# Performance work log

Hardware: AMD Instinct MI355X
Metric: run time of the kernel (lower is better)

Reference implementation:

```python
import jax, jax.numpy as jnp
import numpy as np


def _conv(x, k, pad):
    # x: [B,1,H,W], k: [1,1,kh,kw]
    return jax.lax.conv_general_dilated(
        x, k, window_strides=(1, 1), padding=[(pad, pad), (pad, pad)],
        dimension_numbers=('NCHW', 'OIHW', 'NCHW'))


def _gauss_kernel(size=15, sigma=2.0):
    c = np.arange(size, dtype=np.float32) - size // 2
    k = np.exp(-(c[:, None] ** 2 + c[None, :] ** 2) / (2.0 * sigma ** 2))
    k = k / k.sum()
    return jnp.asarray(k, dtype=jnp.float32)[None, None]


_SOBEL_X = jnp.array([[[[-1., 0., 1.], [-2., 0., 2.], [-1., 0., 1.]]]], dtype=jnp.float32)
_SOBEL_Y = jnp.array([[[[-1., -2., -1.], [0., 0., 0.], [1., 2., 1.]]]], dtype=jnp.float32)
_GAUSS = _gauss_kernel(15, 2.0)


def _edge_density(img):
    gray = 0.299 * img[:, 0] + 0.587 * img[:, 1] + 0.114 * img[:, 2]  # [B,H,W]
    box = jnp.ones((1, 1, 5, 5), jnp.float32) / 25.0  # avg_pool2d, count_include_pad
    blurred = _conv(gray[:, None], box, 2)
    gx = _conv(blurred, _SOBEL_X, 1)
    gy = _conv(blurred, _SOBEL_Y, 1)
    mag = jnp.sqrt(gx ** 2 + gy ** 2)
    hi = mag.max() * 0.2
    lo = hi * 0.3
    edge_map = ((mag > lo) & (mag < hi)).astype(jnp.float32)
    return _conv(edge_map, _GAUSS, 7)  # [B,1,H,W]


def _color_sparsity(img):
    # Replaces the O(K*B*H*W) python loop over unique quantized colors with a
    # 32^3-bin histogram (scatter-add) and a single per-pixel gather.
    b, c, h, w = img.shape
    idx = jnp.clip(jnp.round(img * 31.0), 0, 31).astype(jnp.int32)  # [B,3,H,W]
    code = idx[:, 0] * 1024 + idx[:, 1] * 32 + idx[:, 2]  # [B,H,W]
    counts = jnp.zeros(32 * 32 * 32, jnp.float32).at[code.reshape(-1)].add(1.0)
    prob = counts[code] / float(b * h * w)  # [B,H,W]
    return (-jnp.log(prob + 1e-9) * 1.5)[:, None]  # [B,1,H,W]


def setup_inputs() -> dict:
    key = jax.random.key(0)
    img = jax.random.uniform(key, (1, 3, 3072, 3072), dtype=jnp.float32)
    return {
        'img': img,
        'alpha': jnp.asarray(0.5, dtype=jnp.float32),
        'beta': jnp.asarray(0.5, dtype=jnp.float32),
    }


def reference(img, alpha, beta):
    ed = _edge_density(img)
    cs = _color_sparsity(img)
    en = (ed - ed.min()) / (ed.max() - ed.min() + 1e-9)
    cn = (cs - cs.min()) / (cs.max() - cs.min() + 1e-9)
    return jax.nn.sigmoid(alpha * en + beta * cn)  # [B,1,H,W]
```

## Files before the change

kernel.cpp:

```cpp
#include <hip/hip_runtime.h>
#include <math.h>

#define TW 3072
#define TH 3072
#define NPIX (TW*TH)

__device__ __forceinline__ int qcode(float r, float g, float b) {
    int ir = min(max((int)rintf(__fmul_rn(r, 31.f)), 0), 31);
    int ig = min(max((int)rintf(__fmul_rn(g, 31.f)), 0), 31);
    int ib = min(max((int)rintf(__fmul_rn(b, 31.f)), 0), 31);
    return ir * 1024 + ig * 32 + ib;
}

__device__ __forceinline__ float grayf(float r, float g, float b) {
    return __fadd_rn(__fadd_rn(__fmul_rn(0.299f, r), __fmul_rn(0.587f, g)),
                     __fmul_rn(0.114f, b));
}

__global__ __launch_bounds__(1024) void k_pre(const float4* __restrict__ img4,
                                              float4* __restrict__ gray4,
                                              ushort4* __restrict__ code4,
                                              unsigned* __restrict__ parthist,
                                              unsigned* __restrict__ scal) {
    if (blockIdx.x == 0 && threadIdx.x == 0) {
        scal[0] = 0u;
        scal[1] = 0x7F800000u;
        scal[2] = 0u;
        scal[3] = 0u;
        scal[4] = 0xFFFFFFFFu;
    }
    __shared__ unsigned lh[16384];
    for (int t = threadIdx.x; t < 16384; t += 1024) lh[t] = 0u;
    __syncthreads();
    const int total4 = NPIX / 4;
    const int stride = 256 * 1024;
    int base = blockIdx.x * 1024 + threadIdx.x;
#pragma unroll
    for (int k = 0; k < 8; k += 2) {
        int p = base + k * stride;
        int q = p + stride;
        float4 r0 = img4[p], g0 = img4[p + total4], b0 = img4[p + 2 * total4];
        float4 r1 = img4[q], g1 = img4[q + total4], b1 = img4[q + 2 * total4];
        float4 gy0, gy1;
        gy0.x = grayf(r0.x, g0.x, b0.x); gy0.y = grayf(r0.y, g0.y, b0.y);
        gy0.z = grayf(r0.z, g0.z, b0.z); gy0.w = grayf(r0.w, g0.w, b0.w);
        gy1.x = grayf(r1.x, g1.x, b1.x); gy1.y = grayf(r1.y, g1.y, b1.y);
        gy1.z = grayf(r1.z, g1.z, b1.z); gy1.w = grayf(r1.w, g1.w, b1.w);
        gray4[p] = gy0;
        gray4[q] = gy1;
        int c0 = qcode(r0.x, g0.x, b0.x), c1 = qcode(r0.y, g0.y, b0.y);
        int c2 = qcode(r0.z, g0.z, b0.z), c3 = qcode(r0.w, g0.w, b0.w);
        int d0 = qcode(r1.x, g1.x, b1.x), d1 = qcode(r1.y, g1.y, b1.y);
        int d2 = qcode(r1.z, g1.z, b1.z), d3 = qcode(r1.w, g1.w, b1.w);
        atomicAdd(&lh[c0 >> 1], (c0 & 1) ? 0x10000u : 1u);
        atomicAdd(&lh[c1 >> 1], (c1 & 1) ? 0x10000u : 1u);
        atomicAdd(&lh[c2 >> 1], (c2 & 1) ? 0x10000u : 1u);
        atomicAdd(&lh[c3 >> 1], (c3 & 1) ? 0x10000u : 1u);
        atomicAdd(&lh[d0 >> 1], (d0 & 1) ? 0x10000u : 1u);
        atomicAdd(&lh[d1 >> 1], (d1 & 1) ? 0x10000u : 1u);
        atomicAdd(&lh[d2 >> 1], (d2 & 1) ? 0x10000u : 1u);
        atomicAdd(&lh[d3 >> 1], (d3 & 1) ? 0x10000u : 1u);
        ushort4 cc, dd;
        cc.x = (unsigned short)c0; cc.y = (unsigned short)c1;
        cc.z = (unsigned short)c2; cc.w = (unsigned short)c3;
        dd.x = (unsigned short)d0; dd.y = (unsigned short)d1;
        dd.z = (unsigned short)d2; dd.w = (unsigned short)d3;
        code4[p] = cc;
        code4[q] = dd;
    }
    {
        int p = base + 8 * stride;
        float4 r = img4[p], g = img4[p + total4], b = img4[p + 2 * total4];
        float4 gy;
        gy.x = grayf(r.x, g.x, b.x); gy.y = grayf(r.y, g.y, b.y);
        gy.z = grayf(r.z, g.z, b.z); gy.w = grayf(r.w, g.w, b.w);
        gray4[p] = gy;
        int c0 = qcode(r.x, g.x, b.x), c1 = qcode(r.y, g.y, b.y);
        int c2 = qcode(r.z, g.z, b.z), c3 = qcode(r.w, g.w, b.w);
        atomicAdd(&lh[c0 >> 1], (c0 & 1) ? 0x10000u : 1u);
        atomicAdd(&lh[c1 >> 1], (c1 & 1) ? 0x10000u : 1u);
        atomicAdd(&lh[c2 >> 1], (c2 & 1) ? 0x10000u : 1u);
        atomicAdd(&lh[c3 >> 1], (c3 & 1) ? 0x10000u : 1u);
        ushort4 cc;
        cc.x = (unsigned short)c0; cc.y = (unsigned short)c1;
        cc.z = (unsigned short)c2; cc.w = (unsigned short)c3;
        code4[p] = cc;
    }
    __syncthreads();
    unsigned* dst = parthist + (size_t)blockIdx.x * 16384;
    for (int t = threadIdx.x; t < 16384; t += 1024) dst[t] = lh[t];
}

__global__ void k_reduce(const unsigned* __restrict__ parthist, unsigned* __restrict__ hist,
                         float* __restrict__ cstab, unsigned* __restrict__ scal) {
    int b = blockIdx.x * blockDim.x + threadIdx.x;
    unsigned lo = 0u, hi = 0u;
#pragma unroll 4
    for (int k = 0; k < 256; k++) {
        unsigned v = parthist[(size_t)k * 16384 + b];
        lo += v & 0xFFFFu;
        hi += v >> 16;
    }
    hist[2 * b] = lo;
    hist[2 * b + 1] = hi;
    const float N = (float)NPIX;
    cstab[2 * b]     = -logf((float)lo / N + 1e-9f) * 1.5f;
    cstab[2 * b + 1] = -logf((float)hi / N + 1e-9f) * 1.5f;
    unsigned mx = max(lo, hi);
    unsigned mn = 0xFFFFFFFFu;
    if (lo) mn = lo;
    if (hi) mn = min(mn, hi);
#pragma unroll
    for (int o = 32; o > 0; o >>= 1) {
        mx = max(mx, (unsigned)__shfl_down((int)mx, o));
        mn = min(mn, (unsigned)__shfl_down((int)mn, o));
    }
    __shared__ unsigned smx[4], smn[4];
    int lane = threadIdx.x & 63, wv = threadIdx.x >> 6;
    if (lane == 0) { smx[wv] = mx; smn[wv] = mn; }
    __syncthreads();
    if (threadIdx.x == 0) {
        unsigned a = max(max(smx[0], smx[1]), max(smx[2], smx[3]));
        unsigned c = min(min(smn[0], smn[1]), min(smn[2], smn[3]));
        atomicMax(&scal[3], a);
        atomicMin(&scal[4], c);
    }
}

__device__ __forceinline__ void blockMaxMinAtomic(float vmax, float vmin,
                                                  unsigned* pmax, unsigned* pmin) {
#pragma unroll
    for (int o = 32; o > 0; o >>= 1) {
        vmax = fmaxf(vmax, __shfl_down(vmax, o));
        vmin = fminf(vmin, __shfl_down(vmin, o));
    }
    __shared__ float smax[8], smin[8];
    int lane = threadIdx.x & 63, wv = threadIdx.x >> 6;
    if (lane == 0) { smax[wv] = vmax; smin[wv] = vmin; }
    __syncthreads();
    if (threadIdx.x == 0) {
        int nw = blockDim.x >> 6;
        float a = smax[0], b = smin[0];
        for (int k = 1; k < nw; k++) { a = fmaxf(a, smax[k]); b = fminf(b, smin[k]); }
        if (pmax) atomicMax(pmax, __float_as_uint(a));
        if (pmin) atomicMin(pmin, __float_as_uint(b));
    }
}

#define BS_W 256
#define BS_H 24
#define GTW 264
#define GTH 30
#define BLW 260
#define BLH 26
__global__ __launch_bounds__(512) void k_boxsobel(const float* __restrict__ g,
                                                  float* __restrict__ mag,
                                                  unsigned* __restrict__ scal) {
    __shared__ float GT[GTH * GTW];
    __shared__ float BL[BLH * BLW];
    int tid = threadIdx.x;
    int x0 = blockIdx.x * BS_W;
    int y0 = blockIdx.y * BS_H;
    for (int t = tid; t < GTH * GTW; t += 512) {
        int ly = t / GTW, lx = t - ly * GTW;
        int y = y0 - 3 + ly, x = x0 - 3 + lx;
        GT[t] = ((unsigned)y < TH && (unsigned)x < TW) ? g[(size_t)y * TW + x] : 0.f;
    }
    __syncthreads();
    for (int t = tid; t < BLH * 65; t += 512) {
        int by = t / 65, gx = t - by * 65;
        int c0 = gx * 4;
        float acc[4] = {0.f, 0.f, 0.f, 0.f};
#pragma unroll
        for (int a = 0; a < 5; a++) {
            const float* rp = &GT[(by + a) * GTW + c0];
            float4 A = *(const float4*)rp;
            float4 B = *(const float4*)(rp + 4);
            float v[8] = {A.x, A.y, A.z, A.w, B.x, B.y, B.z, B.w};
#pragma unroll
            for (int j = 0; j < 4; j++)
#pragma unroll
                for (int b = 0; b < 5; b++)
                    acc[j] = __fadd_rn(acc[j], __fmul_rn(v[j + b], 0.04f));
        }
        int yb = y0 - 1 + by;
        float4 o;
        float* ov = (float*)&o;
#pragma unroll
        for (int j = 0; j < 4; j++) {
            int xb = x0 - 1 + c0 + j;
            ov[j] = ((unsigned)yb < TH && (unsigned)xb < TW) ? acc[j] : 0.f;
        }
        *(float4*)&BL[by * BLW + c0] = o;
    }
    __syncthreads();
    float tmax = 0.f;
    for (int t = tid; t < 24 * 64; t += 512) {
        int oy = t >> 6, gx = t & 63;
        int c0 = gx * 4;
        float v[3][6];
#pragma unroll
        for (int a = 0; a < 3; a++) {
            const float* rp = &BL[(oy + a) * BLW + c0];
            float4 P = *(const float4*)rp;
            float2 Q = *(const float2*)(rp + 4);
            v[a][0] = P.x; v[a][1] = P.y; v[a][2] = P.z; v[a][3] = P.w;
            v[a][4] = Q.x; v[a][5] = Q.y;
        }
        float4 mo;
        float* mv = (float*)&mo;
#pragma unroll
        for (int j = 0; j < 4; j++) {
            float gxv = 0.f;
            gxv = __fadd_rn(gxv, __fmul_rn(-1.f, v[0][j + 0]));
            gxv = __fadd_rn(gxv, v[0][j + 2]);
            gxv = __fadd_rn(gxv, __fmul_rn(-2.f, v[1][j + 0]));
            gxv = __fadd_rn(gxv, __fmul_rn(2.f, v[1][j + 2]));
            gxv = __fadd_rn(gxv, __fmul_rn(-1.f, v[2][j + 0]));
            gxv = __fadd_rn(gxv, v[2][j + 2]);
            float gyv = 0.f;
            gyv = __fadd_rn(gyv, __fmul_rn(-1.f, v[0][j + 0]));
            gyv = __fadd_rn(gyv, __fmul_rn(-2.f, v[0][j + 1]));
            gyv = __fadd_rn(gyv, __fmul_rn(-1.f, v[0][j + 2]));
            gyv = __fadd_rn(gyv, v[2][j + 0]);
            gyv = __fadd_rn(gyv, __fmul_rn(2.f, v[2][j + 1]));
            gyv = __fadd_rn(gyv, v[2][j + 2]);
            float m = sqrtf(__fadd_rn(__fmul_rn(gxv, gxv), __fmul_rn(gyv, gyv)));
            mv[j] = m;
            tmax = fmaxf(tmax, m);
        }
        *(float4*)&mag[(size_t)(y0 + oy) * TW + x0 + c0] = mo;
    }
    blockMaxMinAtomic(tmax, 0.f, &scal[0], nullptr);
}

#define GS_W 256
#define GS_H 48
#define E_H 62
#define EWB 10
__global__ __launch_bounds__(512) void k_gauss(const float* __restrict__ mag,
                                               float* __restrict__ ed,
                                               const unsigned* __restrict__ scal,
                                               unsigned* __restrict__ scalw) {
    __shared__ float wt[15];
    __shared__ unsigned E8[E_H * EWB];
    __shared__ float EH[E_H * GS_W];
    if (threadIdx.x == 0) {
        float w[15];
        float s = 0.f;
        for (int t = 0; t < 15; t++) {
            int c = t - 7;
            w[t] = expf(-(float)(c * c) * 0.125f);
            s += w[t];
        }
        for (int t = 0; t < 15; t++) wt[t] = w[t] / s;
    }
    __syncthreads();
    float magmax = __uint_as_float(scal[0]);
    float hi = __fmul_rn(magmax, 0.2f);
    float lo = __fmul_rn(hi, 0.3f);
    int tid = threadIdx.x;
    int lane = tid & 63, wave = tid >> 6;
    int x0 = blockIdx.x * GS_W;
    int y0 = blockIdx.y * GS_H;
    for (int item = wave; item < E_H * 5; item += 8) {
        int ly = item / 5, ch = item - ly * 5;
        int y = y0 - 7 + ly;
        int lx = ch * 64 + lane;
        int x = x0 - 7 + lx;
        float m = ((unsigned)y < TH && lx < 270 && (unsigned)x < TW)
                      ? mag[(size_t)y * TW + x] : 0.f;
        unsigned long long mask = __ballot(m > lo && m < hi);
        if (lane < 2) E8[ly * EWB + ch * 2 + lane] = (unsigned)(mask >> (32 * lane));
    }
    __syncthreads();
    for (int t = tid; t < E_H * 64; t += 512) {
        int ly = t >> 6, gx = t & 63;
        int c0 = gx * 4;
        int w0 = c0 >> 5, sh = c0 & 31;
        unsigned lo32 = E8[ly * EWB + w0];
        unsigned hi32 = E8[ly * EWB + w0 + 1];
        unsigned long long win = (((unsigned long long)hi32 << 32) | lo32) >> sh;
        float e[18];
#pragma unroll
        for (int j = 0; j < 18; j++) e[j] = (float)((unsigned)(win >> j) & 1u);
        float4 o;
        float* ov = (float*)&o;
#pragma unroll
        for (int j = 0; j < 4; j++) {
            float acc = 0.f;
#pragma unroll
            for (int k = 0; k < 15; k++) acc = fmaf(e[j + k], wt[k], acc);
            ov[j] = acc;
        }
        *(float4*)&EH[ly * GS_W + c0] = o;
    }
    __syncthreads();
    float tmin = INFINITY, tmax = 0.f;
    for (int t = tid; t < GS_H * 64; t += 512) {
        int r = t >> 6, gx = t & 63;
        int c0 = gx * 4;
        float a0 = 0.f, a1 = 0.f, a2 = 0.f, a3 = 0.f;
#pragma unroll
        for (int k = 0; k < 15; k++) {
            float4 v = *(const float4*)&EH[(r + k) * GS_W + c0];
            a0 = fmaf(v.x, wt[k], a0);
            a1 = fmaf(v.y, wt[k], a1);
            a2 = fmaf(v.z, wt[k], a2);
            a3 = fmaf(v.w, wt[k], a3);
        }
        float4 o; o.x = a0; o.y = a1; o.z = a2; o.w = a3;
        *(float4*)&ed[(size_t)(y0 + r) * TW + x0 + c0] = o;
        tmin = fminf(tmin, fminf(fminf(a0, a1), fminf(a2, a3)));
        tmax = fmaxf(tmax, fmaxf(fmaxf(a0, a1), fmaxf(a2, a3)));
    }
    blockMaxMinAtomic(tmax, tmin, &scalw[2], &scalw[1]);
}

__global__ void k_final(float4* __restrict__ io4, const ushort4* __restrict__ code4,
                        const float* __restrict__ cstab, const unsigned* __restrict__ scal,
                        const float* __restrict__ alphap, const float* __restrict__ betap) {
    float edmin = __uint_as_float(scal[1]);
    float edmax = __uint_as_float(scal[2]);
    float edrange = edmax - edmin + 1e-9f;
    const float N = (float)NPIX;
    float csmin = -logf((float)scal[3] / N + 1e-9f) * 1.5f;
    float csmax = -logf((float)scal[4] / N + 1e-9f) * 1.5f;
    float csrange = csmax - csmin + 1e-9f;
    float alpha = *alphap, beta = *betap;
    const int total4 = NPIX / 4;
    int stride = gridDim.x * blockDim.x;
    for (int p = blockIdx.x * blockDim.x + threadIdx.x; p < total4; p += stride) {
        float4 ed = io4[p];
        ushort4 cc = code4[p];
        float edv[4] = {ed.x, ed.y, ed.z, ed.w};
        unsigned short cv[4] = {cc.x, cc.y, cc.z, cc.w};
        float ov[4];
#pragma unroll
        for (int t = 0; t < 4; t++) {
            float en = (edv[t] - edmin) / edrange;
            float cs = cstab[cv[t]];
            float cn = (cs - csmin) / csrange;
            float x = alpha * en + beta * cn;
            ov[t] = 1.f / (1.f + expf(-x));
        }
        float4 o;
        o.x = ov[0]; o.y = ov[1]; o.z = ov[2]; o.w = ov[3];
        io4[p] = o;
    }
}

extern "C" void kernel_launch(void* const* d_in, const int* in_sizes, int n_in,
                              void* d_out, int out_size, void* d_ws, size_t ws_size,
                              hipStream_t stream) {
    const float* img = (const float*)d_in[0];
    const float* alphap = (const float*)d_in[1];
    const float* betap = (const float*)d_in[2];
    float* out = (float*)d_out;

    char* ws = (char*)d_ws;
    unsigned* scal = (unsigned*)ws;
    unsigned* hist = (unsigned*)(ws + 1024);
    float* cstab = (float*)(ws + 1024 + 131072);
    float* G = (float*)(ws + 524288);
    float* M = (float*)(ws + 524288 + (size_t)NPIX * 4);
    unsigned short* code = (unsigned short*)(ws + 524288 + (size_t)NPIX * 8);
    unsigned* parthist = (unsigned*)M;

    hipLaunchKernelGGL(k_pre, dim3(256), dim3(1024), 0, stream,
                       (const float4*)img, (float4*)G, (ushort4*)code, parthist, scal);
    hipLaunchKernelGGL(k_reduce, dim3(64), dim3(256), 0, stream, parthist, hist, cstab, scal);
    hipLaunchKernelGGL(k_boxsobel, dim3(TW / BS_W, TH / BS_H), dim3(512), 0, stream,
                       G, M, scal);
    hipLaunchKernelGGL(k_gauss, dim3(TW / GS_W, TH / GS_H), dim3(512), 0, stream,
                       M, out, scal, scal);
    hipLaunchKernelGGL(k_final, dim3(2304), dim3(256), 0, stream, (float4*)out,
                       (const ushort4*)code, cstab, scal, alphap, betap);
}
```

Baseline: 336.2 us.

## Parallelize histogram reduce, add quantized color table in LDS, shrink stencil tiles

```diff
diff --git a/kernel.cpp b/kernel.cpp
--- a/kernel.cpp
+++ b/kernel.cpp
@@ -91,40 +91,55 @@
     for (int t = threadIdx.x; t < 16384; t += 1024) dst[t] = lh[t];
 }
 
-__global__ void k_reduce(const unsigned* __restrict__ parthist, unsigned* __restrict__ hist,
-                         float* __restrict__ cstab, unsigned* __restrict__ scal) {
-    int b = blockIdx.x * blockDim.x + threadIdx.x;
+__global__ __launch_bounds__(1024) void k_reduce(const unsigned* __restrict__ parthist,
+                                                 float* __restrict__ cstab,
+                                                 unsigned* __restrict__ scal) {
+    __shared__ unsigned slo[1024], shi[1024];
+    int tid = threadIdx.x;
+    int tsub = tid >> 6;
+    int pl = tid & 63;
+    int b = blockIdx.x * 64 + pl;
     unsigned lo = 0u, hi = 0u;
-#pragma unroll 4
-    for (int k = 0; k < 256; k++) {
-        unsigned v = parthist[(size_t)k * 16384 + b];
+#pragma unroll
+    for (int j = 0; j < 16; j++) {
+        unsigned v = parthist[(size_t)(tsub * 16 + j) * 16384 + b];
         lo += v & 0xFFFFu;
         hi += v >> 16;
     }
-    hist[2 * b] = lo;
-    hist[2 * b + 1] = hi;
+    slo[tid] = lo;
+    shi[tid] = hi;
+    __syncthreads();
+    if (tid < 64) {
+        unsigned Lo = 0u, Hi = 0u;
+#pragma unroll
+        for (int t = 0; t < 16; t++) { Lo += slo[t * 64 + tid]; Hi += shi[t * 64 + tid]; }
+        const float N = (float)NPIX;
+        int bb = blockIdx.x * 64 + tid;
+        cstab[2 * bb]     = -logf((float)Lo / N + 1e-9f) * 1.5f;
+        cstab[2 * bb + 1] = -logf((float)Hi / N + 1e-9f) * 1.5f;
+        unsigned mx = max(Lo, Hi);
+        unsigned mn = 0xFFFFFFFFu;
+        if (Lo) mn = Lo;
+        if (Hi) mn = min(mn, Hi);
+#pragma unroll
+        for (int o = 32; o > 0; o >>= 1) {
+            mx = max(mx, (unsigned)__shfl_down((int)mx, o));
+            mn = min(mn, (unsigned)__shfl_down((int)mn, o));
+        }
+        if (tid == 0) { atomicMax(&scal[3], mx); atomicMin(&scal[4], mn); }
+    }
+}
+
+__global__ void k_tab(const float* __restrict__ cstab, const unsigned* __restrict__ scal,
+                      unsigned short* __restrict__ cn16) {
+    int b = blockIdx.x * 256 + threadIdx.x;
     const float N = (float)NPIX;
-    cstab[2 * b]     = -logf((float)lo / N + 1e-9f) * 1.5f;
-    cstab[2 * b + 1] = -logf((float)hi / N + 1e-9f) * 1.5f;
-    unsigned mx = max(lo, hi);
-    unsigned mn = 0xFFFFFFFFu;
-    if (lo) mn = lo;
-    if (hi) mn = min(mn, hi);
-#pragma unroll
-    for (int o = 32; o > 0; o >>= 1) {
-        mx = max(mx, (unsigned)__shfl_down((int)mx, o));
-        mn = min(mn, (unsigned)__shfl_down((int)mn, o));
-    }
-    __shared__ unsigned smx[4], smn[4];
-    int lane = threadIdx.x & 63, wv = threadIdx.x >> 6;
-    if (lane == 0) { smx[wv] = mx; smn[wv] = mn; }
-    __syncthreads();
-    if (threadIdx.x == 0) {
-        unsigned a = max(max(smx[0], smx[1]), max(smx[2], smx[3]));
-        unsigned c = min(min(smn[0], smn[1]), min(smn[2], smn[3]));
-        atomicMax(&scal[3], a);
-        atomicMin(&scal[4], c);
-    }
+    float csmin = -logf((float)scal[3] / N + 1e-9f) * 1.5f;
+    float csmax = -logf((float)scal[4] / N + 1e-9f) * 1.5f;
+    float csrange = csmax - csmin + 1e-9f;
+    float cn = (cstab[b] - csmin) / csrange;
+    int q = (int)rintf(cn * 65535.f);
+    cn16[b] = (unsigned short)min(max(q, 0), 65535);
 }
 
 __device__ __forceinline__ void blockMaxMinAtomic(float vmax, float vmin,
@@ -148,14 +163,14 @@
 }
 
 #define BS_W 256
-#define BS_H 24
+#define BS_H 16
 #define GTW 264
-#define GTH 30
+#define GTH 22
 #define BLW 260
-#define BLH 26
-__global__ __launch_bounds__(512) void k_boxsobel(const float* __restrict__ g,
-                                                  float* __restrict__ mag,
-                                                  unsigned* __restrict__ scal) {
+#define BLH 18
+__global__ __launch_bounds__(512, 6) void k_boxsobel(const float* __restrict__ g,
+                                                     float* __restrict__ mag,
+                                                     unsigned* __restrict__ scal) {
     __shared__ float GT[GTH * GTW];
     __shared__ float BL[BLH * BLW];
     int tid = threadIdx.x;
@@ -195,7 +210,7 @@
     }
     __syncthreads();
     float tmax = 0.f;
-    for (int t = tid; t < 24 * 64; t += 512) {
+    for (int t = tid; t < BS_H * 64; t += 512) {
         int oy = t >> 6, gx = t & 63;
         int c0 = gx * 4;
         float v[3][6];
@@ -235,13 +250,13 @@
 }
 
 #define GS_W 256
-#define GS_H 48
-#define E_H 62
+#define GS_H 32
+#define E_H 46
 #define EWB 10
-__global__ __launch_bounds__(512) void k_gauss(const float* __restrict__ mag,
-                                               float* __restrict__ ed,
-                                               const unsigned* __restrict__ scal,
-                                               unsigned* __restrict__ scalw) {
+__global__ __launch_bounds__(512, 6) void k_gauss(const float* __restrict__ mag,
+                                                  float* __restrict__ ed,
+                                                  const unsigned* __restrict__ scal,
+                                                  unsigned* __restrict__ scalw) {
     __shared__ float wt[15];
     __shared__ unsigned E8[E_H * EWB];
     __shared__ float EH[E_H * GS_W];
@@ -317,30 +332,32 @@
     blockMaxMinAtomic(tmax, tmin, &scalw[2], &scalw[1]);
 }
 
-__global__ void k_final(float4* __restrict__ io4, const ushort4* __restrict__ code4,
-                        const float* __restrict__ cstab, const unsigned* __restrict__ scal,
-                        const float* __restrict__ alphap, const float* __restrict__ betap) {
+__global__ __launch_bounds__(1024) void k_final(float4* __restrict__ io4,
+                                                const ushort4* __restrict__ code4,
+                                                const unsigned* __restrict__ cn16w,
+                                                const unsigned* __restrict__ scal,
+                                                const float* __restrict__ alphap,
+                                                const float* __restrict__ betap) {
+    __shared__ unsigned short cnS[32768];
+    unsigned* cnS32 = (unsigned*)cnS;
+    for (int t = threadIdx.x; t < 16384; t += 1024) cnS32[t] = cn16w[t];
     float edmin = __uint_as_float(scal[1]);
     float edmax = __uint_as_float(scal[2]);
     float edrange = edmax - edmin + 1e-9f;
-    const float N = (float)NPIX;
-    float csmin = -logf((float)scal[3] / N + 1e-9f) * 1.5f;
-    float csmax = -logf((float)scal[4] / N + 1e-9f) * 1.5f;
-    float csrange = csmax - csmin + 1e-9f;
     float alpha = *alphap, beta = *betap;
+    __syncthreads();
     const int total4 = NPIX / 4;
     int stride = gridDim.x * blockDim.x;
     for (int p = blockIdx.x * blockDim.x + threadIdx.x; p < total4; p += stride) {
-        float4 ed = io4[p];
+        float4 edv4 = io4[p];
         ushort4 cc = code4[p];
-        float edv[4] = {ed.x, ed.y, ed.z, ed.w};
+        float edv[4] = {edv4.x, edv4.y, edv4.z, edv4.w};
         unsigned short cv[4] = {cc.x, cc.y, cc.z, cc.w};
         float ov[4];
 #pragma unroll
         for (int t = 0; t < 4; t++) {
             float en = (edv[t] - edmin) / edrange;
-            float cs = cstab[cv[t]];
-            float cn = (cs - csmin) / csrange;
+            float cn = (float)cnS[cv[t]] * (1.f / 65535.f);
             float x = alpha * en + beta * cn;
             ov[t] = 1.f / (1.f + expf(-x));
         }
@@ -360,7 +377,7 @@
 
     char* ws = (char*)d_ws;
     unsigned* scal = (unsigned*)ws;
-    unsigned* hist = (unsigned*)(ws + 1024);
+    unsigned short* cn16 = (unsigned short*)(ws + 1024);
     float* cstab = (float*)(ws + 1024 + 131072);
     float* G = (float*)(ws + 524288);
     float* M = (float*)(ws + 524288 + (size_t)NPIX * 4);
@@ -369,11 +386,12 @@
 
     hipLaunchKernelGGL(k_pre, dim3(256), dim3(1024), 0, stream,
                        (const float4*)img, (float4*)G, (ushort4*)code, parthist, scal);
-    hipLaunchKernelGGL(k_reduce, dim3(64), dim3(256), 0, stream, parthist, hist, cstab, scal);
+    hipLaunchKernelGGL(k_reduce, dim3(256), dim3(1024), 0, stream, parthist, cstab, scal);
+    hipLaunchKernelGGL(k_tab, dim3(128), dim3(256), 0, stream, cstab, scal, cn16);
     hipLaunchKernelGGL(k_boxsobel, dim3(TW / BS_W, TH / BS_H), dim3(512), 0, stream,
                        G, M, scal);
     hipLaunchKernelGGL(k_gauss, dim3(TW / GS_W, TH / GS_H), dim3(512), 0, stream,
                        M, out, scal, scal);
-    hipLaunchKernelGGL(k_final, dim3(2304), dim3(256), 0, stream, (float4*)out,
-                       (const ushort4*)code, cstab, scal, alphap, betap);
-}
+    hipLaunchKernelGGL(k_final, dim3(512), dim3(1024), 0, stream, (float4*)out,
+                       (const ushort4*)code, (const unsigned*)cn16, scal, alphap, betap);
+}
```

Result: faster. 320.0 us (-4.8%).
